# Optimization experiments

Hardware: AMD Instinct MI355X
Metric: run time of the kernel (lower is better)

## Reference

```python
import jax, jax.numpy as jnp
import numpy as np

B, H, W, C_IN, C_HID = 32, 64, 64, 384, 128

def setup_inputs() -> dict:
    key = jax.random.key(0)
    k0, k1, k2 = jax.random.split(key, 3)
    dino_features = jax.random.normal(k0, (B, H, W, C_IN), dtype=jnp.float32)
    # Xavier-uniform(gain=0.5) bounds for conv weights, HWIO layout
    fan1 = C_IN * 9 + C_HID * 9
    lim1 = 0.5 * np.sqrt(6.0 / fan1)
    W1 = jax.random.uniform(k1, (3, 3, C_IN, C_HID), minval=-lim1, maxval=lim1, dtype=jnp.float32)
    b1 = jnp.zeros((C_HID,), dtype=jnp.float32)
    fan2 = C_HID + 1
    lim2 = 0.5 * np.sqrt(6.0 / fan2)
    W2 = jax.random.uniform(k2, (1, 1, C_HID, 1), minval=-lim2, maxval=lim2, dtype=jnp.float32)
    b2 = jnp.zeros((1,), dtype=jnp.float32)
    return {"dino_features": dino_features, "W1": W1, "b1": b1, "W2": W2, "b2": b2}

def _conv(x, w, pad):
    # x: NHWC, w: HWIO -> NHWC
    return jax.lax.conv_general_dilated(
        x, w, window_strides=(1, 1), padding=pad,
        dimension_numbers=("NHWC", "HWIO", "NHWC"))

def reference(dino_features, W1, b1, W2, b2):
    # conv3x3 (pad 1) -> ReLU -> conv1x1 -> sigmoid; output (B,H,W,1)
    h = jax.nn.relu(_conv(dino_features, W1, ((1, 1), (1, 1))) + b1)
    logits = _conv(h, W2, ((0, 0), (0, 0))) + b2
    return jax.nn.sigmoid(logits)
```

## Files before the change

### kernel.cpp

```cpp
#include <hip/hip_runtime.h>
#include <hip/hip_bf16.h>
#include <math.h>


typedef __attribute__((ext_vector_type(8))) unsigned short ushort8;
typedef __attribute__((ext_vector_type(8))) __bf16 bf16x8;
typedef __attribute__((ext_vector_type(4))) float floatx4;

static __device__ __forceinline__ unsigned short f2bf_rne(float f) {
  union { float f; unsigned int u; } x; x.f = f;
  unsigned int u = x.u;
  return (unsigned short)((u + 0x7fffu + ((u >> 16) & 1u)) >> 16);
}

static __device__ __forceinline__ ushort8 pack8(const float* v) {
  ushort8 r;
#pragma unroll
  for (int i = 0; i < 4; ++i) {
    __hip_bfloat162 p = __float22bfloat162_rn(make_float2(v[2 * i], v[2 * i + 1]));
    union { __hip_bfloat162 b; unsigned int u; } c;
    c.b = p;
    r[2 * i] = (unsigned short)(c.u & 0xffffu);
    r[2 * i + 1] = (unsigned short)(c.u >> 16);
  }
  return r;
}

__global__ void prep_w1_kernel(const float* __restrict__ W1,
                               unsigned short* __restrict__ W1b) {
  __shared__ unsigned short tile[32 * 128];
  const int kk = blockIdx.x;
  const int o = kk / 12;
  const int chunk = kk - o * 12;
  const float* src = W1 + (o * 384 + chunk * 32) * 128;
  const int t = threadIdx.x;
#pragma unroll
  for (int i = 0; i < 16; ++i) {
    int idx = t + i * 256;
    int c = idx >> 7;
    int n = idx & 127;
    tile[n * 32 + c] = f2bf_rne(src[idx]);
  }
  __syncthreads();
  unsigned short* dst = W1b + kk * 4096;
#pragma unroll
  for (int i = 0; i < 16; ++i) {
    int idx = t + i * 256;
    dst[idx] = tile[idx];
  }
}

__global__ __launch_bounds__(256) void conv_fused_kernel(
    const float* __restrict__ x, const unsigned short* __restrict__ W1b,
    const float* __restrict__ b1, const float* __restrict__ W2,
    const float* __restrict__ b2, float* __restrict__ out) {
  __shared__ alignas(16) unsigned short Ah[180 * 40];
  __shared__ float hsum[128 * 4];

  const int t = threadIdx.x;
  const int w = t >> 6;
  const int lane = t & 63;
  const int g = lane >> 4;
  const int lr = lane & 15;

  const int img = blockIdx.x >> 5;
  const int tileId = blockIdx.x & 31;
  const int ty0 = (tileId >> 2) << 3;
  const int tx0 = (tileId & 3) << 4;

  int svalid[3];
  const float* sptr[3];
  int sloff[3];
  const bool act2 = t < 208;
#pragma unroll
  for (int j = 0; j < 3; ++j) {
    int i = t + j * 256;
    int px = i >> 2, sub = i & 3;
    int hy = (px * 57) >> 10;
    int hx = px - hy * 18;
    int iy = ty0 + hy - 1, ix = tx0 + hx - 1;
    int v = ((unsigned)iy < 64u) && ((unsigned)ix < 64u);
    if (j == 2 && !act2) v = 0;
    svalid[j] = v;
    int iyc = v ? iy : 0, ixc = v ? ix : 0;
    sptr[j] = x + ((((img << 6) + iyc) << 6) + ixc) * 384 + sub * 8;
    sloff[j] = px * 40 + sub * 8;
  }

  const int boff = ((w * 32 + lr) << 5) + (g << 3);
  const int aoffl = lr * 40 + (g << 3);

  floatx4 acc[8][2] = {};

  const float b1v0 = b1[w * 32 + lr];
  const float b1v1 = b1[w * 32 + 16 + lr];
  const float w2v0 = W2[w * 32 + lr];
  const float w2v1 = W2[w * 32 + 16 + lr];

  float sreg[3][8];

#pragma unroll
  for (int j = 0; j < 3; ++j) {
    if (svalid[j]) {
      *(float4*)&sreg[j][0] = *(const float4*)sptr[j];
      *(float4*)&sreg[j][4] = *(const float4*)(sptr[j] + 4);
    } else {
#pragma unroll
      for (int e = 0; e < 8; ++e) sreg[j][e] = 0.0f;
    }
  }

  for (int chunk = 0; chunk < 12; ++chunk) {
    __syncthreads();
    *(ushort8*)&Ah[sloff[0]] = pack8(sreg[0]);
    *(ushort8*)&Ah[sloff[1]] = pack8(sreg[1]);
    if (act2) *(ushort8*)&Ah[sloff[2]] = pack8(sreg[2]);
    __syncthreads();

    if (chunk < 11) {
      const int off = (chunk + 1) << 5;
#pragma unroll
      for (int j = 0; j < 3; ++j) {
        if (svalid[j]) {
          *(float4*)&sreg[j][0] = *(const float4*)(sptr[j] + off);
          *(float4*)&sreg[j][4] = *(const float4*)(sptr[j] + off + 4);
        }
      }
    }

#pragma unroll
    for (int ox = 0; ox < 3; ++ox) {
      bf16x8 bf[3][2];
#pragma unroll
      for (int oy = 0; oy < 3; ++oy) {
        const unsigned short* bp =
            W1b + ((((oy * 3 + ox) * 12 + chunk) << 12)) + boff;
        bf[oy][0] = *(const bf16x8*)bp;
        bf[oy][1] = *(const bf16x8*)(bp + 512);
      }
#pragma unroll
      for (int h = 0; h < 10; ++h) {
        const bf16x8 af = *(const bf16x8*)&Ah[h * 720 + ox * 40 + aoffl];
#pragma unroll
        for (int oy = 0; oy < 3; ++oy) {
          const int mi = h - oy;
          if (mi >= 0 && mi < 8) {
            acc[mi][0] = __builtin_amdgcn_mfma_f32_16x16x32_bf16(
                af, bf[oy][0], acc[mi][0], 0, 0, 0);
            acc[mi][1] = __builtin_amdgcn_mfma_f32_16x16x32_bf16(
                af, bf[oy][1], acc[mi][1], 0, 0, 0);
          }
        }
      }
    }
  }

#pragma unroll
  for (int mi = 0; mi < 8; ++mi) {
#pragma unroll
    for (int r = 0; r < 4; ++r) {
      float h0 = fmaxf(acc[mi][0][r] + b1v0, 0.0f);
      float h1 = fmaxf(acc[mi][1][r] + b1v1, 0.0f);
      float v = h0 * w2v0 + h1 * w2v1;
      v += __shfl_xor(v, 1);
      v += __shfl_xor(v, 2);
      v += __shfl_xor(v, 4);
      v += __shfl_xor(v, 8);
      if (lr == 0) {
        int m = mi * 16 + g * 4 + r;
        hsum[m * 4 + w] = v;
      }
    }
  }
  __syncthreads();
  if (t < 128) {
    float s = hsum[t * 4 + 0] + hsum[t * 4 + 1] + hsum[t * 4 + 2] +
              hsum[t * 4 + 3] + b2[0];
    float sig = 1.0f / (1.0f + expf(-s));
    int prow = t >> 4, pcol = t & 15;
    out[((((img << 6) + ty0 + prow) << 6) + tx0 + pcol)] = sig;
  }
}

extern "C" void kernel_launch(void* const* d_in, const int* in_sizes, int n_in,
                              void* d_out, int out_size, void* d_ws, size_t ws_size,
                              hipStream_t stream) {
  const float* x  = (const float*)d_in[0];
  const float* W1 = (const float*)d_in[1];
  const float* b1 = (const float*)d_in[2];
  const float* W2 = (const float*)d_in[3];
  const float* b2 = (const float*)d_in[4];
  float* out = (float*)d_out;
  unsigned short* W1b = (unsigned short*)d_ws;

  prep_w1_kernel<<<108, 256, 0, stream>>>(W1, W1b);
  conv_fused_kernel<<<1024, 256, 0, stream>>>(x, W1b, b1, W2, b2, out);
}
```

Measured before the change: 346.6 us.

## Double-buffer LDS input tile and prefetch two chunks ahead

Result: slower. 448.9 us (+29.5%).

```diff
diff --git a/kernel.cpp b/kernel.cpp
--- a/kernel.cpp
+++ b/kernel.cpp
@@ -50,11 +50,11 @@
   }
 }
 
-__global__ __launch_bounds__(256) void conv_fused_kernel(
+__global__ __launch_bounds__(256, 4) void conv_fused_kernel(
     const float* __restrict__ x, const unsigned short* __restrict__ W1b,
     const float* __restrict__ b1, const float* __restrict__ W2,
     const float* __restrict__ b2, float* __restrict__ out) {
-  __shared__ alignas(16) unsigned short Ah[180 * 40];
+  __shared__ alignas(16) unsigned short Ah[2 * 7200];
   __shared__ float hsum[128 * 4];
 
   const int t = threadIdx.x;
@@ -69,7 +69,7 @@
   const int tx0 = (tileId & 3) << 4;
 
   int svalid[3];
-  const float* sptr[3];
+  int soff[3];
   int sloff[3];
   const bool act2 = t < 208;
 #pragma unroll
@@ -83,7 +83,7 @@
     if (j == 2 && !act2) v = 0;
     svalid[j] = v;
     int iyc = v ? iy : 0, ixc = v ? ix : 0;
-    sptr[j] = x + ((((img << 6) + iyc) << 6) + ixc) * 384 + sub * 8;
+    soff[j] = ((((img << 6) + iyc) << 6) + ixc) * 384 + sub * 8;
     sloff[j] = px * 40 + sub * 8;
   }
 
@@ -98,34 +98,38 @@
   const float w2v1 = W2[w * 32 + 16 + lr];
 
   float sreg[3][8];
+#pragma unroll
+  for (int j = 0; j < 3; ++j)
+#pragma unroll
+    for (int e = 0; e < 8; ++e) sreg[j][e] = 0.0f;
 
 #pragma unroll
   for (int j = 0; j < 3; ++j) {
     if (svalid[j]) {
-      *(float4*)&sreg[j][0] = *(const float4*)sptr[j];
-      *(float4*)&sreg[j][4] = *(const float4*)(sptr[j] + 4);
-    } else {
-#pragma unroll
-      for (int e = 0; e < 8; ++e) sreg[j][e] = 0.0f;
-    }
-  }
-
-  for (int chunk = 0; chunk < 12; ++chunk) {
-    __syncthreads();
-    *(ushort8*)&Ah[sloff[0]] = pack8(sreg[0]);
-    *(ushort8*)&Ah[sloff[1]] = pack8(sreg[1]);
-    if (act2) *(ushort8*)&Ah[sloff[2]] = pack8(sreg[2]);
-    __syncthreads();
-
-    if (chunk < 11) {
-      const int off = (chunk + 1) << 5;
-#pragma unroll
-      for (int j = 0; j < 3; ++j) {
-        if (svalid[j]) {
-          *(float4*)&sreg[j][0] = *(const float4*)(sptr[j] + off);
-          *(float4*)&sreg[j][4] = *(const float4*)(sptr[j] + off + 4);
-        }
-      }
+      *(float4*)&sreg[j][0] = *(const float4*)(x + soff[j]);
+      *(float4*)&sreg[j][4] = *(const float4*)(x + soff[j] + 4);
+    }
+  }
+  *(ushort8*)&Ah[sloff[0]] = pack8(sreg[0]);
+  *(ushort8*)&Ah[sloff[1]] = pack8(sreg[1]);
+  if (act2) *(ushort8*)&Ah[sloff[2]] = pack8(sreg[2]);
+#pragma unroll
+  for (int j = 0; j < 3; ++j) {
+    if (svalid[j]) {
+      *(float4*)&sreg[j][0] = *(const float4*)(x + soff[j] + 32);
+      *(float4*)&sreg[j][4] = *(const float4*)(x + soff[j] + 36);
+    }
+  }
+  __syncthreads();
+
+  for (int c = 0; c < 12; ++c) {
+    const int rb = (c & 1) * 7200;
+    const int wb = 7200 - rb;
+
+    if (c < 11) {
+      *(ushort8*)&Ah[wb + sloff[0]] = pack8(sreg[0]);
+      *(ushort8*)&Ah[wb + sloff[1]] = pack8(sreg[1]);
+      if (act2) *(ushort8*)&Ah[wb + sloff[2]] = pack8(sreg[2]);
     }
 
 #pragma unroll
@@ -134,13 +138,23 @@
 #pragma unroll
       for (int oy = 0; oy < 3; ++oy) {
         const unsigned short* bp =
-            W1b + ((((oy * 3 + ox) * 12 + chunk) << 12)) + boff;
+            W1b + ((((oy * 3 + ox) * 12 + c) << 12)) + boff;
         bf[oy][0] = *(const bf16x8*)bp;
         bf[oy][1] = *(const bf16x8*)(bp + 512);
       }
+      if (ox == 2 && c < 10) {
+        const int off = (c + 2) << 5;
+#pragma unroll
+        for (int j = 0; j < 3; ++j) {
+          if (svalid[j]) {
+            *(float4*)&sreg[j][0] = *(const float4*)(x + soff[j] + off);
+            *(float4*)&sreg[j][4] = *(const float4*)(x + soff[j] + off + 4);
+          }
+        }
+      }
 #pragma unroll
       for (int h = 0; h < 10; ++h) {
-        const bf16x8 af = *(const bf16x8*)&Ah[h * 720 + ox * 40 + aoffl];
+        const bf16x8 af = *(const bf16x8*)&Ah[rb + h * 720 + ox * 40 + aoffl];
 #pragma unroll
         for (int oy = 0; oy < 3; ++oy) {
           const int mi = h - oy;
@@ -153,6 +167,7 @@
         }
       }
     }
+    __syncthreads();
   }
 
 #pragma unroll
```
